# Optimization experiments

Hardware: AMD Instinct MI355X
Metric: run time of the kernel (lower is better)

## Reference

```python
import jax, jax.numpy as jnp
import numpy as np

K = 3          # kernel_size
EPS = 1e-12    # epsilon from l2_normal and abs-clamp


def setup_inputs() -> dict:
    key = jax.random.key(0)
    k1, k2 = jax.random.split(key)
    B, H, W, C, F = 8, 224, 224, 32, 32
    image = jax.random.normal(k1, (B, H, W, C), dtype=jnp.float32)
    # glorot-uniform-ish weight, shape (1, C*K*K, filters)
    fan = C * K * K + F
    lim = np.sqrt(6.0 / fan).astype(np.float32)
    w = jax.random.uniform(k2, (1, C * K * K, F), dtype=jnp.float32, minval=-lim, maxval=lim)
    p = jnp.full((F,), 100.0 ** 0.5, dtype=jnp.float32)   # p init = sqrt(100)
    q = jnp.full((1,), 10.0 ** 0.5, dtype=jnp.float32)    # q init = sqrt(10)
    return {"image": image, "w": w, "p": p, "q": q}


def reference(image, w, p, q):
    # CosSim2D, kernel_size=3, stride=1, padding='same', non-depthwise.
    B, H, W, C = image.shape
    pad = K // 2
    padded = jnp.pad(image, ((0, 0), (pad, pad), (pad, pad), (0, 0)))
    # im2col: kernel-position-major, channel-minor -> matches tf.stack(axis=3) + reshape
    patches = jnp.stack(
        [padded[:, dy:dy + H, dx:dx + W, :] for dy in range(K) for dx in range(K)],
        axis=3,
    )  # (B, H, W, K*K, C)
    x = patches.reshape(B, H * W, K * K * C)
    q_term = jnp.square(q) / 10.0                       # scalar (broadcast)
    x_norm = jnp.sqrt(jnp.maximum(jnp.sum(x * x, axis=2, keepdims=True), EPS)) + q_term
    w_norm = jnp.sqrt(jnp.maximum(jnp.sum(w * w, axis=1, keepdims=True), EPS)) + q_term
    sim = jnp.matmul(x / x_norm, (w / w_norm)[0])       # (B, H*W, filters)
    out = jnp.sign(sim) * jnp.power(jnp.abs(sim) + EPS, jnp.square(p) / 100.0)
    return out.reshape(B, H, W, -1)
```

## Files before the change

kernel.cpp:

```cpp
#include <hip/hip_runtime.h>
#include <hip/hip_bf16.h>


#define H_ 224
#define W_ 224
#define C_ 32
#define F_ 32

#define NSTEP 18
#define HROWS 10
#define HCOLS 34
#define SLOTS (HROWS * HCOLS * 8)

typedef __bf16 bf16_t;
typedef bf16_t bf16x8 __attribute__((ext_vector_type(8)));
typedef float f32x16 __attribute__((ext_vector_type(16)));

#define WFRAG_BYTES (NSTEP * 64 * 8 * 2)

__global__ __launch_bounds__(256) void cos2d_prep(
    const float* __restrict__ w, const float* __restrict__ p,
    const float* __restrict__ q, bf16_t* __restrict__ wfrag,
    float* __restrict__ winv, float* __restrict__ ef) {
  const int tid = threadIdx.x;
  if (blockIdx.x == 0) {
    __shared__ float part[8][32];
    const int f = tid & 31, kg = tid >> 5;
    float s = 0.f;
#pragma unroll
    for (int i = 0; i < 36; ++i) {
      const float v = w[(kg + 8 * i) * F_ + f];
      s += v * v;
    }
    part[kg][f] = s;
    __syncthreads();
    if (tid < 32) {
      float t = 0.f;
#pragma unroll
      for (int g = 0; g < 8; ++g) t += part[g][tid];
      const float qt = q[0] * q[0] * 0.1f;
      winv[tid] = 1.f / (sqrtf(fmaxf(t, 1e-12f)) + qt);
      ef[tid] = p[tid] * p[tid] * 0.01f;
    }
  } else {
    const int t = (blockIdx.x - 1) * 256 + tid;
    if (t < NSTEP * 64) {
      const int s2 = t >> 6, l = t & 63;
      const int ff = l & 31;
      union { bf16_t v[8]; uint4 u; } tv;
#pragma unroll
      for (int e = 0; e < 8; ++e) {
        const int kk = s2 * 16 + ((l >> 5) << 3) + e;
        tv.v[e] = (bf16_t)w[kk * F_ + ff];
      }
      *(uint4*)(wfrag + (size_t)t * 8) = tv.u;
    }
  }
}

__global__ __launch_bounds__(256, 5) void cos2d_main(
    const float* __restrict__ img, const bf16_t* __restrict__ wfrag,
    const float* __restrict__ winv, const float* __restrict__ ef,
    const float* __restrict__ q, float* __restrict__ out) {
  __shared__ bf16_t xt[HROWS][HCOLS][40];
  __shared__ float ssum[HROWS][HCOLS];

  const int tid = threadIdx.x;
  const int lane = tid & 63;
  const int wv = tid >> 6;
  const int lp = lane & 31;

  const int bid = blockIdx.x;
  const int tw = bid % 7;
  const int th = (bid / 7) % 28;
  const int b  = bid / 196;
  const int h0 = th * 8, w0 = tw * 32;

  const float qt = q[0] * q[0] * 0.1f;
  const float efv = ef[lp];
  const float wnv = winv[lp];
  const bool allfast = __all(__builtin_fabsf(efv - 1.0f) < 1e-6f);

  for (int idx = tid; idx < SLOTS; idx += 256) {
    const int pp = idx >> 3, sub = idx & 7;
    const int rr = pp / HCOLS, cc = pp - rr * HCOLS;
    const int hh = h0 - 1 + rr, wc = w0 - 1 + cc;
    float4 v = make_float4(0.f, 0.f, 0.f, 0.f);
    if ((unsigned)hh < H_ && (unsigned)wc < W_)
      v = *(const float4*)(img + ((size_t)(b * H_ + hh) * W_ + wc) * C_ + sub * 4);
    float s = v.x * v.x + v.y * v.y + v.z * v.z + v.w * v.w;
    s += __shfl_xor(s, 1);
    s += __shfl_xor(s, 2);
    s += __shfl_xor(s, 4);
    union { bf16_t h[4]; uint2 u; } pk;
    pk.h[0] = (bf16_t)v.x; pk.h[1] = (bf16_t)v.y;
    pk.h[2] = (bf16_t)v.z; pk.h[3] = (bf16_t)v.w;
    *(uint2*)&xt[rr][cc][sub * 4] = pk.u;
    if (sub == 0) ssum[rr][cc] = s;
  }
  __syncthreads();

  const int mr0 = wv * 2;

  float xinv[2];
#pragma unroll
  for (int t = 0; t < 2; ++t) {
    const int mr = mr0 + t;
    const float xn2 =
        ssum[mr + 0][lp] + ssum[mr + 0][lp + 1] + ssum[mr + 0][lp + 2] +
        ssum[mr + 1][lp] + ssum[mr + 1][lp + 1] + ssum[mr + 1][lp + 2] +
        ssum[mr + 2][lp] + ssum[mr + 2][lp + 1] + ssum[mr + 2][lp + 2];
    xinv[t] = 1.f / (sqrtf(fmaxf(xn2, 1e-12f)) + qt);
  }

  f32x16 acc0, acc1;
#pragma unroll
  for (int i = 0; i < 16; ++i) { acc0[i] = 0.f; acc1[i] = 0.f; }

  const bf16x8* wf4 = (const bf16x8*)wfrag;
#pragma unroll
  for (int s2 = 0; s2 < NSTEP; ++s2) {
    const bf16x8 bf = wf4[s2 * 64 + lane];
    const int pos = s2 >> 1;
    const int dy = pos / 3, dx = pos - dy * 3;
    const int chof = (s2 & 1) * 16 + ((lane >> 5) << 3);
    const bf16x8 a0 = *(const bf16x8*)&xt[mr0 + 0 + dy][lp + dx][chof];
    const bf16x8 a1 = *(const bf16x8*)&xt[mr0 + 1 + dy][lp + dx][chof];
    acc0 = __builtin_amdgcn_mfma_f32_32x32x16_bf16(a0, bf, acc0, 0, 0, 0);
    acc1 = __builtin_amdgcn_mfma_f32_32x32x16_bf16(a1, bf, acc1, 0, 0, 0);
  }

#pragma unroll
  for (int t = 0; t < 2; ++t) {
    const f32x16& acc = t ? acc1 : acc0;
    const int obase = (b * H_ + h0 + mr0 + t) * W_ + w0;
    if (allfast) {
#pragma unroll
      for (int jj = 0; jj < 16; ++jj) {
        const int row = (jj & 3) + 8 * (jj >> 2) + 4 * (lane >> 5);
        const float xi = __shfl(xinv[t], row);
        const float sim = acc[jj] * xi * wnv;
        const float r = copysignf(fabsf(sim) + 1e-12f, sim);
        __builtin_nontemporal_store(r, &out[(size_t)(obase + row) * F_ + lp]);
      }
    } else {
#pragma unroll
      for (int jj = 0; jj < 16; ++jj) {
        const int row = (jj & 3) + 8 * (jj >> 2) + 4 * (lane >> 5);
        const float xi = __shfl(xinv[t], row);
        const float sim = acc[jj] * xi * wnv;
        const float ps = fabsf(sim) + 1e-12f;
        float r = exp2f(efv * __log2f(ps));
        r = copysignf(r, sim);
        __builtin_nontemporal_store(r, &out[(size_t)(obase + row) * F_ + lp]);
      }
    }
  }
}

extern "C" void kernel_launch(void* const* d_in, const int* in_sizes, int n_in,
                              void* d_out, int out_size, void* d_ws, size_t ws_size,
                              hipStream_t stream) {
  const float* img = (const float*)d_in[0];
  const float* w   = (const float*)d_in[1];
  const float* p   = (const float*)d_in[2];
  const float* q   = (const float*)d_in[3];

  bf16_t* wfrag = (bf16_t*)d_ws;
  float*  winv  = (float*)((char*)d_ws + WFRAG_BYTES);
  float*  ef    = winv + 64;

  cos2d_prep<<<6, 256, 0, stream>>>(w, p, q, wfrag, winv, ef);
  cos2d_main<<<1568, 256, 0, stream>>>(img, wfrag, winv, ef, q, (float*)d_out);
}
```

Baseline: 34.54 us.

## Give each wave a private halo tile to drop the block barrier

Each wave now stages its own 4-row halo strip into a per-wave shared-memory region and reads only from it, so the block-wide __syncthreads is removed and waves proceed independently. The cost is redundant loading: halo rows shared between neighbouring waves are fetched twice (16 rows instead of 10 per block), and shared-memory use grows, lowering the occupancy hint from 5 to 3 blocks. The intent is to overlap load and MFMA phases across waves instead of stalling on a barrier.

```diff
diff --git a/kernel.cpp b/kernel.cpp
--- a/kernel.cpp
+++ b/kernel.cpp
@@ -8,9 +8,10 @@
 #define F_ 32
 
 #define NSTEP 18
-#define HROWS 10
+#define WROWS 4
 #define HCOLS 34
-#define SLOTS (HROWS * HCOLS * 8)
+#define WSLOTS (WROWS * HCOLS * 8)
+#define WITER (WSLOTS / 64)
 
 typedef __bf16 bf16_t;
 typedef bf16_t bf16x8 __attribute__((ext_vector_type(8)));
@@ -58,12 +59,12 @@
   }
 }
 
-__global__ __launch_bounds__(256, 5) void cos2d_main(
+__global__ __launch_bounds__(256, 3) void cos2d_main(
     const float* __restrict__ img, const bf16_t* __restrict__ wfrag,
     const float* __restrict__ winv, const float* __restrict__ ef,
     const float* __restrict__ q, float* __restrict__ out) {
-  __shared__ bf16_t xt[HROWS][HCOLS][40];
-  __shared__ float ssum[HROWS][HCOLS];
+  __shared__ bf16_t xt[4][WROWS][HCOLS][40];
+  __shared__ float ssum[4][WROWS][HCOLS];
 
   const int tid = threadIdx.x;
   const int lane = tid & 63;
@@ -74,14 +75,17 @@
   const int tw = bid % 7;
   const int th = (bid / 7) % 28;
   const int b  = bid / 196;
-  const int h0 = th * 8, w0 = tw * 32;
+  const int h0 = th * 8 + wv * 2;
+  const int w0 = tw * 32;
 
   const float qt = q[0] * q[0] * 0.1f;
   const float efv = ef[lp];
   const float wnv = winv[lp];
   const bool allfast = __all(__builtin_fabsf(efv - 1.0f) < 1e-6f);
 
-  for (int idx = tid; idx < SLOTS; idx += 256) {
+#pragma unroll
+  for (int i = 0; i < WITER; ++i) {
+    const int idx = lane + 64 * i;
     const int pp = idx >> 3, sub = idx & 7;
     const int rr = pp / HCOLS, cc = pp - rr * HCOLS;
     const int hh = h0 - 1 + rr, wc = w0 - 1 + cc;
@@ -95,21 +99,17 @@
     union { bf16_t h[4]; uint2 u; } pk;
     pk.h[0] = (bf16_t)v.x; pk.h[1] = (bf16_t)v.y;
     pk.h[2] = (bf16_t)v.z; pk.h[3] = (bf16_t)v.w;
-    *(uint2*)&xt[rr][cc][sub * 4] = pk.u;
-    if (sub == 0) ssum[rr][cc] = s;
+    *(uint2*)&xt[wv][rr][cc][sub * 4] = pk.u;
+    if (sub == 0) ssum[wv][rr][cc] = s;
   }
-  __syncthreads();
-
-  const int mr0 = wv * 2;
 
   float xinv[2];
 #pragma unroll
   for (int t = 0; t < 2; ++t) {
-    const int mr = mr0 + t;
     const float xn2 =
-        ssum[mr + 0][lp] + ssum[mr + 0][lp + 1] + ssum[mr + 0][lp + 2] +
-        ssum[mr + 1][lp] + ssum[mr + 1][lp + 1] + ssum[mr + 1][lp + 2] +
-        ssum[mr + 2][lp] + ssum[mr + 2][lp + 1] + ssum[mr + 2][lp + 2];
+        ssum[wv][t + 0][lp] + ssum[wv][t + 0][lp + 1] + ssum[wv][t + 0][lp + 2] +
+        ssum[wv][t + 1][lp] + ssum[wv][t + 1][lp + 1] + ssum[wv][t + 1][lp + 2] +
+        ssum[wv][t + 2][lp] + ssum[wv][t + 2][lp + 1] + ssum[wv][t + 2][lp + 2];
     xinv[t] = 1.f / (sqrtf(fmaxf(xn2, 1e-12f)) + qt);
   }
 
@@ -124,8 +124,8 @@
     const int pos = s2 >> 1;
     const int dy = pos / 3, dx = pos - dy * 3;
     const int chof = (s2 & 1) * 16 + ((lane >> 5) << 3);
-    const bf16x8 a0 = *(const bf16x8*)&xt[mr0 + 0 + dy][lp + dx][chof];
-    const bf16x8 a1 = *(const bf16x8*)&xt[mr0 + 1 + dy][lp + dx][chof];
+    const bf16x8 a0 = *(const bf16x8*)&xt[wv][0 + dy][lp + dx][chof];
+    const bf16x8 a1 = *(const bf16x8*)&xt[wv][1 + dy][lp + dx][chof];
     acc0 = __builtin_amdgcn_mfma_f32_32x32x16_bf16(a0, bf, acc0, 0, 0, 0);
     acc1 = __builtin_amdgcn_mfma_f32_32x32x16_bf16(a1, bf, acc1, 0, 0, 0);
   }
@@ -133,7 +133,7 @@
 #pragma unroll
   for (int t = 0; t < 2; ++t) {
     const f32x16& acc = t ? acc1 : acc0;
-    const int obase = (b * H_ + h0 + mr0 + t) * W_ + w0;
+    const int obase = (b * H_ + h0 + t) * W_ + w0;
     if (allfast) {
 #pragma unroll
       for (int jj = 0; jj < 16; ++jj) {
```

Result: slower. 45.01 us (+30.3%).

## Stage image tile via direct global-to-LDS DMA and compute norms from LDS

Applied to the files above, without the earlier changes.

Replaces the register round-trip staging (load float4, convert to bf16, shuffle-reduce squares) with global_load_lds DMA of raw fp32 granules into an XOR-swizzled LDS tile. Conversion to bf16 and the squared-norm accumulation move into the MFMA loop, which reuses each loaded A fragment across three dy taps. Weight fragments are preloaded into registers. This doubles the LDS footprint (fp32 instead of bf16), so the occupancy hint drops from 5 to 3 blocks, and it raises register pressure in exchange for cutting staging instructions.

```diff
diff --git a/kernel.cpp b/kernel.cpp
--- a/kernel.cpp
+++ b/kernel.cpp
@@ -10,13 +10,21 @@
 #define NSTEP 18
 #define HROWS 10
 #define HCOLS 34
-#define SLOTS (HROWS * HCOLS * 8)
+#define NPIX (HROWS * HCOLS)
+#define NGRAN (NPIX * 8)
+#define NGRAN_PAD 2816
 
 typedef __bf16 bf16_t;
 typedef bf16_t bf16x8 __attribute__((ext_vector_type(8)));
 typedef float f32x16 __attribute__((ext_vector_type(16)));
 
 #define WFRAG_BYTES (NSTEP * 64 * 8 * 2)
+
+__device__ __forceinline__ void dma16(const void* gp, void* lp) {
+  __builtin_amdgcn_global_load_lds(
+      (const __attribute__((address_space(1))) void*)gp,
+      (__attribute__((address_space(3))) void*)lp, 16, 0, 0);
+}
 
 __global__ __launch_bounds__(256) void cos2d_prep(
     const float* __restrict__ w, const float* __restrict__ p,
@@ -58,17 +66,17 @@
   }
 }
 
-__global__ __launch_bounds__(256, 5) void cos2d_main(
+__global__ __launch_bounds__(256, 3) void cos2d_main(
     const float* __restrict__ img, const bf16_t* __restrict__ wfrag,
     const float* __restrict__ winv, const float* __restrict__ ef,
     const float* __restrict__ q, float* __restrict__ out) {
-  __shared__ bf16_t xt[HROWS][HCOLS][40];
-  __shared__ float ssum[HROWS][HCOLS];
+  __shared__ __align__(16) float xt[NGRAN_PAD * 4];
 
   const int tid = threadIdx.x;
   const int lane = tid & 63;
   const int wv = tid >> 6;
   const int lp = lane & 31;
+  const int hi2 = (lane >> 5) * 2;
 
   const int bid = blockIdx.x;
   const int tw = bid % 7;
@@ -81,54 +89,74 @@
   const float wnv = winv[lp];
   const bool allfast = __all(__builtin_fabsf(efv - 1.0f) < 1e-6f);
 
-  for (int idx = tid; idx < SLOTS; idx += 256) {
-    const int pp = idx >> 3, sub = idx & 7;
-    const int rr = pp / HCOLS, cc = pp - rr * HCOLS;
-    const int hh = h0 - 1 + rr, wc = w0 - 1 + cc;
-    float4 v = make_float4(0.f, 0.f, 0.f, 0.f);
-    if ((unsigned)hh < H_ && (unsigned)wc < W_)
-      v = *(const float4*)(img + ((size_t)(b * H_ + hh) * W_ + wc) * C_ + sub * 4);
-    float s = v.x * v.x + v.y * v.y + v.z * v.z + v.w * v.w;
-    s += __shfl_xor(s, 1);
-    s += __shfl_xor(s, 2);
-    s += __shfl_xor(s, 4);
-    union { bf16_t h[4]; uint2 u; } pk;
-    pk.h[0] = (bf16_t)v.x; pk.h[1] = (bf16_t)v.y;
-    pk.h[2] = (bf16_t)v.z; pk.h[3] = (bf16_t)v.w;
-    *(uint2*)&xt[rr][cc][sub * 4] = pk.u;
-    if (sub == 0) ssum[rr][cc] = s;
+  bf16x8 bfrag[NSTEP];
+  const bf16x8* wf4 = (const bf16x8*)wfrag;
+#pragma unroll
+  for (int s2 = 0; s2 < NSTEP; ++s2) bfrag[s2] = wf4[s2 * 64 + lane];
+
+#pragma unroll
+  for (int k = 0; k < 11; ++k) {
+    const int s = k * 256 + tid;
+    float* lb = &xt[(k * 256 + wv * 64) * 4];
+    if (s < NGRAN) {
+      const int pp = s >> 3;
+      const int c  = (s & 7) ^ (pp & 7);
+      const int rr = pp / HCOLS, cc = pp - rr * HCOLS;
+      const int hh = h0 - 1 + rr, wc = w0 - 1 + cc;
+      if ((unsigned)hh < H_ && (unsigned)wc < W_) {
+        dma16(img + ((size_t)(b * H_ + hh) * W_ + wc) * C_ + c * 4, lb);
+      } else {
+        *(float4*)&xt[(size_t)s * 4] = make_float4(0.f, 0.f, 0.f, 0.f);
+      }
+    }
   }
   __syncthreads();
 
   const int mr0 = wv * 2;
 
+  f32x16 acc0, acc1;
+#pragma unroll
+  for (int i = 0; i < 16; ++i) { acc0[i] = 0.f; acc1[i] = 0.f; }
+  float psum[4] = {0.f, 0.f, 0.f, 0.f};
+
+#pragma unroll
+  for (int h = 0; h < 2; ++h) {
+#pragma unroll
+    for (int dx = 0; dx < 3; ++dx) {
+      const int c0 = h * 4 + hi2;
+      bf16x8 af[4];
+#pragma unroll
+      for (int r = 0; r < 4; ++r) {
+        const int p = (mr0 + r) * HCOLS + lp + dx;
+        const int g0 = p * 8 + ((c0 + 0) ^ (p & 7));
+        const int g1 = p * 8 + ((c0 + 1) ^ (p & 7));
+        const float4 f0 = *(const float4*)&xt[(size_t)g0 * 4];
+        const float4 f1 = *(const float4*)&xt[(size_t)g1 * 4];
+        psum[r] += f0.x * f0.x + f0.y * f0.y + f0.z * f0.z + f0.w * f0.w +
+                   f1.x * f1.x + f1.y * f1.y + f1.z * f1.z + f1.w * f1.w;
+        bf16x8 a;
+        a[0] = (bf16_t)f0.x; a[1] = (bf16_t)f0.y;
+        a[2] = (bf16_t)f0.z; a[3] = (bf16_t)f0.w;
+        a[4] = (bf16_t)f1.x; a[5] = (bf16_t)f1.y;
+        a[6] = (bf16_t)f1.z; a[7] = (bf16_t)f1.w;
+        af[r] = a;
+      }
+#pragma unroll
+      for (int dy = 0; dy < 3; ++dy) {
+        const bf16x8 bf = bfrag[2 * (dy * 3 + dx) + h];
+        acc0 = __builtin_amdgcn_mfma_f32_32x32x16_bf16(af[dy],     bf, acc0, 0, 0, 0);
+        acc1 = __builtin_amdgcn_mfma_f32_32x32x16_bf16(af[dy + 1], bf, acc1, 0, 0, 0);
+      }
+    }
+  }
+
+#pragma unroll
+  for (int r = 0; r < 4; ++r) psum[r] += __shfl_xor(psum[r], 32);
+  const float xn2_0 = psum[0] + psum[1] + psum[2];
+  const float xn2_1 = psum[1] + psum[2] + psum[3];
   float xinv[2];
-#pragma unroll
-  for (int t = 0; t < 2; ++t) {
-    const int mr = mr0 + t;
-    const float xn2 =
-        ssum[mr + 0][lp] + ssum[mr + 0][lp + 1] + ssum[mr + 0][lp + 2] +
-        ssum[mr + 1][lp] + ssum[mr + 1][lp + 1] + ssum[mr + 1][lp + 2] +
-        ssum[mr + 2][lp] + ssum[mr + 2][lp + 1] + ssum[mr + 2][lp + 2];
-    xinv[t] = 1.f / (sqrtf(fmaxf(xn2, 1e-12f)) + qt);
-  }
-
-  f32x16 acc0, acc1;
-#pragma unroll
-  for (int i = 0; i < 16; ++i) { acc0[i] = 0.f; acc1[i] = 0.f; }
-
-  const bf16x8* wf4 = (const bf16x8*)wfrag;
-#pragma unroll
-  for (int s2 = 0; s2 < NSTEP; ++s2) {
-    const bf16x8 bf = wf4[s2 * 64 + lane];
-    const int pos = s2 >> 1;
-    const int dy = pos / 3, dx = pos - dy * 3;
-    const int chof = (s2 & 1) * 16 + ((lane >> 5) << 3);
-    const bf16x8 a0 = *(const bf16x8*)&xt[mr0 + 0 + dy][lp + dx][chof];
-    const bf16x8 a1 = *(const bf16x8*)&xt[mr0 + 1 + dy][lp + dx][chof];
-    acc0 = __builtin_amdgcn_mfma_f32_32x32x16_bf16(a0, bf, acc0, 0, 0, 0);
-    acc1 = __builtin_amdgcn_mfma_f32_32x32x16_bf16(a1, bf, acc1, 0, 0, 0);
-  }
+  xinv[0] = 1.f / (sqrtf(fmaxf(xn2_0, 1e-12f)) + qt);
+  xinv[1] = 1.f / (sqrtf(fmaxf(xn2_1, 1e-12f)) + qt);
 
 #pragma unroll
   for (int t = 0; t < 2; ++t) {
```

New measurement: 32.67 us. 5.4% less time.
